# Optimization experiments

Measured on AMD Instinct MI355X. Metric: run time of the kernel, lower is better.

## Reference

```python
import jax, jax.numpy as jnp
import numpy as np
from jax import lax

STRIDES = (8, 16, 32, 64, 128)
LEVEL_HW = ((100, 128), (50, 64), (25, 32), (13, 16), (7, 8))
N, C = 16, 80
IMG_H, IMG_W = 800, 1024
THRESH = 0.05
IOU_THR = 0.6
PRE_NMS_K = 1000
POST_K = 100
CLS_OFFSET = 4096.0  # > max image coord, separates classes for batched NMS


def setup_inputs() -> dict:
    key = jax.random.key(0)
    ks = jax.random.split(key, 15)
    inp = {}
    for l, (h, w) in enumerate(LEVEL_HW):
        inp[f"cls{l}"] = jax.random.normal(ks[3 * l], (N, C, h, w), dtype=jnp.float32)
        # ltrb distances scaled to realistic pixel extents
        inp[f"reg{l}"] = jax.random.uniform(ks[3 * l + 1], (N, 4, h, w), dtype=jnp.float32) * 128.0
        inp[f"ctr{l}"] = jax.random.normal(ks[3 * l + 2], (N, 1, h, w), dtype=jnp.float32)
    return inp


def _level(cls, reg, ctr, stride):
    n, c, h, w = cls.shape
    sx = jnp.arange(w, dtype=jnp.float32) * stride + stride / 2.0
    sy = jnp.arange(h, dtype=jnp.float32) * stride + stride / 2.0
    px = jnp.broadcast_to(sx[None, :], (h, w)).reshape(-1)  # [hw]
    py = jnp.broadcast_to(sy[:, None], (h, w)).reshape(-1)  # [hw]
    # sqrt(cls_prob * centerness_prob), as in the source
    scores = jnp.sqrt(jax.nn.sigmoid(cls) * jax.nn.sigmoid(ctr))  # [n,c,h,w]
    scores = scores.transpose(0, 2, 3, 1).reshape(n, h * w, c)
    regf = reg.transpose(0, 2, 3, 1).reshape(n, h * w, 4)
    vals = scores.max(axis=-1)          # best class score per location
    labels = scores.argmax(axis=-1)
    vals = jnp.where(vals > THRESH, vals, 0.0)  # score threshold (zeroed instead of dropped)
    x1 = jnp.clip(px[None, :] - regf[..., 0], 0.0, IMG_W)
    y1 = jnp.clip(py[None, :] - regf[..., 1], 0.0, IMG_H)
    x2 = jnp.clip(px[None, :] + regf[..., 2], 0.0, IMG_W)
    y2 = jnp.clip(py[None, :] + regf[..., 3], 0.0, IMG_H)
    boxes = jnp.stack([x1, y1, x2, y2], axis=-1)  # [n,hw,4]
    return vals, labels, boxes


def _pairwise_iou(b):  # b: [K,4]
    area = (b[:, 2] - b[:, 0]) * (b[:, 3] - b[:, 1])
    lt = jnp.maximum(b[:, None, :2], b[None, :, :2])
    rb = jnp.minimum(b[:, None, 2:], b[None, :, 2:])
    wh = jnp.clip(rb - lt, 0.0)
    inter = wh[..., 0] * wh[..., 1]
    return inter / (area[:, None] + area[None, :] - inter + 1e-9)


def _nms_single(boxes, scores, labels):
    # class-aware NMS via per-class coordinate offset (torchvision batched_nms trick)
    ob = boxes + (labels.astype(boxes.dtype) * CLS_OFFSET)[:, None]
    iou = _pairwise_iou(ob)  # [K,K]
    K = boxes.shape[0]
    idxs = jnp.arange(K)

    def body(valid, i):
        keep_i = valid[i]
        valid = valid & ~(keep_i & (iou[i] > IOU_THR) & (idxs > i))
        return valid, keep_i

    _, keeps = lax.scan(body, scores > 0.0, idxs)  # greedy, scores already sorted desc
    kept_scores = jnp.where(keeps, scores, 0.0)
    top_vals, top = lax.top_k(kept_scores, POST_K)
    return boxes[top], top_vals, labels[top]


def _forward(levels):
    vals_l, labels_l, boxes_l = [], [], []
    for cls, reg, ctr, stride in levels:
        v, la, b = _level(cls, reg, ctr, stride)
        vals_l.append(v)
        labels_l.append(la)
        boxes_l.append(b)
    scores = jnp.concatenate(vals_l, axis=1)   # [N,P]
    labels = jnp.concatenate(labels_l, axis=1)  # [N,P]
    boxes = jnp.concatenate(boxes_l, axis=1)    # [N,P,4]
    tv, ti = lax.top_k(scores, PRE_NMS_K)       # pre-NMS top-k, sorted desc
    boxes_k = jnp.take_along_axis(boxes, ti[:, :, None], axis=1)
    labels_k = jnp.take_along_axis(labels, ti, axis=1)
    return jax.vmap(_nms_single)(boxes_k, tv, labels_k)


def reference(cls0, reg0, ctr0, cls1, reg1, ctr1, cls2, reg2, ctr2,
              cls3, reg3, ctr3, cls4, reg4, ctr4):
    levels = [
        (cls0, reg0, ctr0, 8), (cls1, reg1, ctr1, 16), (cls2, reg2, ctr2, 32),
        (cls3, reg3, ctr3, 64), (cls4, reg4, ctr4, 128),
    ]
    boxes, scores, labels = _forward(levels)
    return boxes, scores, labels  # [N,100,4], [N,100], [N,100]
```

## Files before the change

### kernel.cpp

```cpp
#include <hip/hip_runtime.h>
#include <stdint.h>

#pragma clang fp contract(off)

#define NB 16
#define NC 80
#define P_TOT 17064
#define P4 (P_TOT / 4)
#define PRE_K 1000
#define POST_K 100

__device__ __forceinline__ float sigmoidf_(float x) {
  return 1.0f / (1.0f + expf(-x));
}

__global__ __launch_bounds__(256, 2) void decode_kernel(
    const float* __restrict__ cls0, const float* __restrict__ reg0, const float* __restrict__ ctr0,
    const float* __restrict__ cls1, const float* __restrict__ reg1, const float* __restrict__ ctr1,
    const float* __restrict__ cls2, const float* __restrict__ reg2, const float* __restrict__ ctr2,
    const float* __restrict__ cls3, const float* __restrict__ reg3, const float* __restrict__ ctr3,
    const float* __restrict__ cls4, const float* __restrict__ reg4, const float* __restrict__ ctr4,
    int* __restrict__ labels, float* __restrict__ boxes,
    unsigned long long* __restrict__ keys)
{
  int quad = blockIdx.x * 64 + (threadIdx.x >> 2);
  int t4 = threadIdx.x & 3;
  int n = blockIdx.y;
  if (quad >= P4) return;
  int p0 = quad * 4;
  int off, wsh, hw; float stride; const float *cls, *reg, *ctr;
  if (p0 < 12800)      { off = 0;     wsh = 7; hw = 12800; stride = 8.f;   cls = cls0; reg = reg0; ctr = ctr0; }
  else if (p0 < 16000) { off = 12800; wsh = 6; hw = 3200;  stride = 16.f;  cls = cls1; reg = reg1; ctr = ctr1; }
  else if (p0 < 16800) { off = 16000; wsh = 5; hw = 800;   stride = 32.f;  cls = cls2; reg = reg2; ctr = ctr2; }
  else if (p0 < 17008) { off = 16800; wsh = 4; hw = 208;   stride = 64.f;  cls = cls3; reg = reg3; ctr = ctr3; }
  else                 { off = 17008; wsh = 3; hw = 56;    stride = 128.f; cls = cls4; reg = reg4; ctr = ctr4; }
  int loc0 = p0 - off;
  int y = loc0 >> wsh;
  int x0 = loc0 & ((1 << wsh) - 1);
  float py = (float)y * stride + 0.5f * stride;

  int c0 = t4 * 20;
  const float* cptr = cls + (size_t)n * NC * hw + (size_t)c0 * hw + loc0;
  float4 cv[20];
  #pragma unroll
  for (int k = 0; k < 20; ++k)
    cv[k] = *reinterpret_cast<const float4*>(cptr + (size_t)k * hw);

  float best[4] = { -3.4e38f, -3.4e38f, -3.4e38f, -3.4e38f };
  int bl[4] = { c0, c0, c0, c0 };
  #pragma unroll
  for (int k = 0; k < 20; ++k) {
    int c = c0 + k;
    if (cv[k].x > best[0]) { best[0] = cv[k].x; bl[0] = c; }
    if (cv[k].y > best[1]) { best[1] = cv[k].y; bl[1] = c; }
    if (cv[k].z > best[2]) { best[2] = cv[k].z; bl[2] = c; }
    if (cv[k].w > best[3]) { best[3] = cv[k].w; bl[3] = c; }
  }
  #pragma unroll
  for (int e = 0; e < 4; ++e) {
    #pragma unroll
    for (int d = 1; d <= 2; d <<= 1) {
      float ob = __shfl_xor(best[e], d);
      int ol = __shfl_xor(bl[e], d);
      if (ob > best[e] || (ob == best[e] && ol < bl[e])) { best[e] = ob; bl[e] = ol; }
    }
  }

  int e = t4;
  int loce = loc0 + e;
  float sctr_e = sigmoidf_(ctr[(size_t)n * hw + loce]);
  const float* rbase = reg + (size_t)n * 4 * hw + loce;
  float dl = rbase[0];
  float dt = rbase[(size_t)hw];
  float dr = rbase[(size_t)2 * hw];
  float db = rbase[(size_t)3 * hw];

  float s = sqrtf(sigmoidf_(best[e]) * sctr_e);
  float val = (s > 0.05f) ? s : 0.0f;
  float px = (float)(x0 + e) * stride + 0.5f * stride;
  float x1 = fminf(fmaxf(px - dl, 0.f), 1024.f);
  float y1 = fminf(fmaxf(py - dt, 0.f), 800.f);
  float x2 = fminf(fmaxf(px + dr, 0.f), 1024.f);
  float y2 = fminf(fmaxf(py + db, 0.f), 800.f);

  size_t o = (size_t)n * P_TOT + p0 + e;
  labels[o] = bl[e];
  *reinterpret_cast<float4*>(boxes + 4 * o) = make_float4(x1, y1, x2, y2);
  keys[o] = ((unsigned long long)__float_as_uint(val) << 32)
          | (unsigned long long)(0xFFFFFFFFu - (unsigned)(p0 + e));
}

__global__ __launch_bounds__(1024) void topgather_kernel(
    const unsigned long long* __restrict__ keys,
    const float* __restrict__ boxes, const int* __restrict__ labels,
    float* __restrict__ tboxes, float* __restrict__ tscores, int* __restrict__ tlabels)
{
  int n = blockIdx.x;
  int tid = threadIdx.x;
  __shared__ unsigned hist[16384];
  __shared__ unsigned A[1024];
  __shared__ unsigned s_d;
  __shared__ unsigned long long skey[2048];

  for (int i = tid; i < 16384; i += 1024) hist[i] = 0;
  skey[tid] = 0ULL;
  skey[tid + 1024] = 0ULL;
  __syncthreads();
  const unsigned long long* bk = keys + (size_t)n * P_TOT;
  for (int p = tid; p < P_TOT; p += 1024) {
    unsigned h = (unsigned)(bk[p] >> 48);
    atomicAdd(&hist[h], 1u);
  }
  __syncthreads();

  unsigned bvs[16];
  unsigned ssum = 0;
  #pragma unroll
  for (int q = 0; q < 16; ++q) { bvs[q] = hist[tid * 16 + q]; ssum += bvs[q]; }
  A[tid] = ssum;
  __syncthreads();
  for (int ofs = 1; ofs < 1024; ofs <<= 1) {
    unsigned v = A[tid];
    if (tid + ofs < 1024) v += A[tid + ofs];
    __syncthreads();
    A[tid] = v;
    __syncthreads();
  }
  unsigned An = (tid < 1023) ? A[tid + 1] : 0u;
  {
    unsigned At = A[tid];
    if (At >= PRE_K && An < PRE_K) {
      unsigned cum = An;
      int d = tid * 16;
      bool done = false;
      #pragma unroll
      for (int b = 15; b >= 0; --b) {
        if (!done) {
          cum += bvs[b];
          if (cum >= PRE_K) { d = tid * 16 + b; done = true; }
        }
      }
      s_d = (unsigned)d;
    }
  }
  __syncthreads();
  unsigned dsel = s_d;
  {
    unsigned cum = An;
    #pragma unroll
    for (int b = 15; b >= 0; --b) {
      unsigned h = (unsigned)(tid * 16 + b);
      if (h >= dsel) hist[h] = cum;
      cum += bvs[b];
    }
  }
  __syncthreads();
  for (int p = tid; p < P_TOT; p += 1024) {
    unsigned long long k = bk[p];
    unsigned h = (unsigned)(k >> 48);
    if (h >= dsel) {
      unsigned slot = atomicAdd(&hist[h], 1u);
      if (slot < 2048) skey[slot] = k;
    }
  }
  __syncthreads();
  for (int k2 = 2; k2 <= 2048; k2 <<= 1) {
    for (int j = k2 >> 1; j > 0; j >>= 1) {
      #pragma unroll
      for (int e = 0; e < 2; ++e) {
        int idx = tid + e * 1024;
        int ixj = idx ^ j;
        if (ixj > idx) {
          unsigned long long a = skey[idx], bb = skey[ixj];
          bool sw = ((idx & k2) == 0) ? (a < bb) : (a > bb);
          if (sw) { skey[idx] = bb; skey[ixj] = a; }
        }
      }
      __syncthreads();
    }
  }
  if (tid < PRE_K) {
    unsigned long long k = skey[tid];
    unsigned idx = 0xFFFFFFFFu - (unsigned)(k & 0xFFFFFFFFu);
    float sc = __uint_as_float((unsigned)(k >> 32));
    size_t src = (size_t)n * P_TOT + idx;
    size_t dst = (size_t)n * PRE_K + tid;
    tscores[dst] = sc;
    tlabels[dst] = labels[src];
    *reinterpret_cast<float4*>(tboxes + 4 * dst) =
        *reinterpret_cast<const float4*>(boxes + 4 * src);
  }
}

__global__ __launch_bounds__(128) void iou_kernel(
    const float* __restrict__ tboxes, const int* __restrict__ tlabels,
    unsigned long long* __restrict__ colsupp)
{
  int jb = blockIdx.x, w = blockIdx.y, n = blockIdx.z;
  int tid = threadIdx.x;
  int j = jb * 128 + tid;
  bool jvalid = (j < PRE_K);
  int ibase = w * 64;

  if (ibase >= jb * 128 + 128) {
    if (jvalid) colsupp[((size_t)n * PRE_K + j) * 16 + w] = 0ULL;
    return;
  }

  __shared__ float4 sb[64];
  __shared__ float sa[64];
  if (tid < 64) {
    int i = ibase + tid;
    float4 v = make_float4(0.f, 0.f, 0.f, 0.f);
    if (i < PRE_K) {
      const float* b = tboxes + ((size_t)n * PRE_K + i) * 4;
      float offv = (float)tlabels[(size_t)n * PRE_K + i] * 4096.0f;
      v = make_float4(b[0] + offv, b[1] + offv, b[2] + offv, b[3] + offv);
    }
    sb[tid] = v;
    sa[tid] = (v.z - v.x) * (v.w - v.y);
  }
  __syncthreads();

  float4 bj = make_float4(0.f, 0.f, 0.f, 0.f);
  if (jvalid) {
    const float* b = tboxes + ((size_t)n * PRE_K + j) * 4;
    float offv = (float)tlabels[(size_t)n * PRE_K + j] * 4096.0f;
    bj = make_float4(b[0] + offv, b[1] + offv, b[2] + offv, b[3] + offv);
  }
  float aj = (bj.z - bj.x) * (bj.w - bj.y);

  unsigned long long m = 0, mb = 0;
  #pragma unroll
  for (int b = 0; b < 64; ++b) {
    float4 bi = sb[b];
    float ai = sa[b];
    float lx = fmaxf(bi.x, bj.x), ly = fmaxf(bi.y, bj.y);
    float rx = fminf(bi.z, bj.z), ry = fminf(bi.w, bj.w);
    float iw = fmaxf(rx - lx, 0.f), ih = fmaxf(ry - ly, 0.f);
    float inter = iw * ih;
    float denom = ai + aj - inter + 1e-9f;
    float t = inter - 0.6f * denom;
    if (t > 0.f) m |= (1ull << b);
    if (fabsf(t) <= denom * 7.62939453125e-6f) mb |= (1ull << b);
  }
  if (mb) {
    unsigned long long r = mb;
    while (r) {
      int b = __ffsll(r) - 1; r &= r - 1;
      float4 bi = sb[b];
      float ai = sa[b];
      float lx = fmaxf(bi.x, bj.x), ly = fmaxf(bi.y, bj.y);
      float rx = fminf(bi.z, bj.z), ry = fminf(bi.w, bj.w);
      float iw = fmaxf(rx - lx, 0.f), ih = fmaxf(ry - ly, 0.f);
      float inter = iw * ih;
      float denom = ai + aj - inter + 1e-9f;
      float iou = inter / denom;
      if (iou > 0.6f) m |= (1ull << b); else m &= ~(1ull << b);
    }
  }
  unsigned long long tri;
  if (ibase >= j) tri = 0ULL;
  else if (j - ibase >= 64) tri = ~0ULL;
  else tri = (1ull << (j - ibase)) - 1ull;
  m &= tri;
  if (jvalid) colsupp[((size_t)n * PRE_K + j) * 16 + w] = m;
}

__global__ __launch_bounds__(1024) void greedyfin_kernel(
    const unsigned long long* __restrict__ colsupp, const float* __restrict__ tscores,
    const float* __restrict__ tboxes, const int* __restrict__ tlabels,
    float* __restrict__ out)
{
  int n = blockIdx.x;
  int tid = threadIdx.x;
  int wave = tid >> 6;
  int lane = tid & 63;
  __shared__ unsigned long long T[136 * 64];
  __shared__ unsigned long long keptw[16];

  {
    int wq = wave;
    int j = wq * 64 + lane;
    int base = (wq * (wq + 1)) / 2;
    if (j < PRE_K) {
      const unsigned long long* C = colsupp + ((size_t)n * PRE_K + j) * 16;
      for (int c = 0; c <= wq; ++c) T[(base + c) * 64 + lane] = C[c];
    } else {
      for (int c = 0; c <= wq; ++c) T[(base + c) * 64 + lane] = 0ULL;
    }
  }
  __syncthreads();

  if (wave == 0) {
    const float* sc = tscores + (size_t)n * PRE_K;
    float sval[16];
    #pragma unroll
    for (int k = 0; k < 16; ++k) {
      int j = k * 64 + lane;
      sval[k] = (j < PRE_K) ? sc[j] : 0.f;
    }
    unsigned removedbits = 0;
    #pragma unroll
    for (int c = 0; c < 16; ++c) {
      unsigned long long col = T[((c * (c + 1)) / 2 + c) * 64 + lane];
      unsigned long long sp = __ballot(sval[c] > 0.f);
      unsigned long long inc = __ballot(((removedbits >> c) & 1u) != 0u);
      unsigned long long K = sp & ~inc;
      unsigned long long kept = 0;
      for (int it = 0; it < 64; ++it) {
        unsigned long long Bsupp = __ballot((col & K) != 0ULL);
        unsigned long long Snew = K & ~Bsupp & ~kept;
        if (Snew == 0ULL) break;
        kept |= Snew;
        unsigned long long Bd = __ballot((col & kept) != 0ULL);
        K &= ~Bd;
      }
      if ((col & kept) != 0ULL) removedbits |= (1u << c);
      #pragma unroll
      for (int w = 0; w < 16; ++w) {
        if (w > c) {
          unsigned long long xw = T[((w * (w + 1)) / 2 + c) * 64 + lane];
          if ((xw & kept) != 0ULL) removedbits |= (1u << w);
        }
      }
      if (lane == 0) keptw[c] = kept;
    }
  }
  __syncthreads();

  __shared__ unsigned sk[1024];
  __shared__ unsigned sz[1024];
  bool inr = (tid < PRE_K);
  bool keep = inr && (((keptw[tid >> 6] >> (tid & 63)) & 1ull) != 0ull);
  sk[tid] = keep ? 1u : 0u;
  sz[tid] = (inr && !keep) ? 1u : 0u;
  __syncthreads();
  for (int ofs = 1; ofs < 1024; ofs <<= 1) {
    unsigned a = (tid >= ofs) ? sk[tid - ofs] : 0;
    unsigned b = (tid >= ofs) ? sz[tid - ofs] : 0;
    __syncthreads();
    sk[tid] += a; sz[tid] += b;
    __syncthreads();
  }
  int nk = (int)sk[1023];
  int slot = -1;
  if (inr) {
    if (keep) {
      int r = (int)sk[tid] - 1;
      if (r < POST_K) slot = r;
    } else {
      int r = nk + (int)sz[tid] - 1;
      if (r < POST_K) slot = r;
    }
  }
  if (slot >= 0) {
    size_t src = (size_t)n * PRE_K + tid;
    size_t ob = ((size_t)n * POST_K + slot) * 4;
    out[ob+0] = tboxes[4*src+0];
    out[ob+1] = tboxes[4*src+1];
    out[ob+2] = tboxes[4*src+2];
    out[ob+3] = tboxes[4*src+3];
    out[(size_t)NB*POST_K*4 + (size_t)n*POST_K + slot] = keep ? tscores[src] : 0.0f;
    out[(size_t)NB*POST_K*5 + (size_t)n*POST_K + slot] = (float)tlabels[src];
  }
}

extern "C" void kernel_launch(void* const* d_in, const int* in_sizes, int n_in,
                              void* d_out, int out_size, void* d_ws, size_t ws_size,
                              hipStream_t stream) {
  char* w = (char*)d_ws;
  auto carve = [&](size_t bytes) { char* p = w; w += (bytes + 255) & ~(size_t)255; return p; };
  int* labels   = (int*)carve((size_t)NB * P_TOT * 4);
  float* boxes  = (float*)carve((size_t)NB * P_TOT * 16);
  unsigned long long* keys = (unsigned long long*)carve((size_t)NB * P_TOT * 8);
  unsigned long long* colsupp = (unsigned long long*)carve((size_t)NB * PRE_K * 16 * 8);
  float* tboxes  = (float*)carve((size_t)NB * PRE_K * 16);
  float* tscores = (float*)carve((size_t)NB * PRE_K * 4);
  int* tlabels   = (int*)carve((size_t)NB * PRE_K * 4);

  const float* cls0 = (const float*)d_in[0];
  const float* reg0 = (const float*)d_in[1];
  const float* ctr0 = (const float*)d_in[2];
  const float* cls1 = (const float*)d_in[3];
  const float* reg1 = (const float*)d_in[4];
  const float* ctr1 = (const float*)d_in[5];
  const float* cls2 = (const float*)d_in[6];
  const float* reg2 = (const float*)d_in[7];
  const float* ctr2 = (const float*)d_in[8];
  const float* cls3 = (const float*)d_in[9];
  const float* reg3 = (const float*)d_in[10];
  const float* ctr3 = (const float*)d_in[11];
  const float* cls4 = (const float*)d_in[12];
  const float* reg4 = (const float*)d_in[13];
  const float* ctr4 = (const float*)d_in[14];

  dim3 dg((P4 + 63) / 64, NB);
  decode_kernel<<<dg, 256, 0, stream>>>(cls0, reg0, ctr0, cls1, reg1, ctr1,
                                        cls2, reg2, ctr2, cls3, reg3, ctr3,
                                        cls4, reg4, ctr4,
                                        labels, boxes, keys);
  topgather_kernel<<<NB, 1024, 0, stream>>>(keys, boxes, labels,
                                            tboxes, tscores, tlabels);
  dim3 gi(8, 16, NB);
  iou_kernel<<<gi, 128, 0, stream>>>(tboxes, tlabels, colsupp);
  greedyfin_kernel<<<NB, 1024, 0, stream>>>(colsupp, tscores, tboxes, tlabels, (float*)d_out);
}
```

Baseline: 83.05 us.

## Replace bitonic sort with bucketed rank placement and wave-shuffle scan in top-k

The top-k gather kernel now computes the histogram suffix sum with wavefront shuffles plus a tiny cross-wave step, replacing the shared-memory Hillis-Steele scan and its many barriers. The full 2048-element bitonic sort is dropped. Bucket start offsets are packed into the histogram entries, and each selected key finds its final position by counting the larger keys within its own bucket. This removes dozens of block-wide sync stages, at the risk of long serial rank loops if one bucket holds many keys, for example the zero-score bucket.

```diff
diff --git a/kernel.cpp b/kernel.cpp
--- a/kernel.cpp
+++ b/kernel.cpp
@@ -97,14 +97,14 @@
 {
   int n = blockIdx.x;
   int tid = threadIdx.x;
+  int wave = tid >> 6;
+  int lane = tid & 63;
   __shared__ unsigned hist[16384];
-  __shared__ unsigned A[1024];
-  __shared__ unsigned s_d;
+  __shared__ unsigned Wt[16], Wsuf[16];
+  __shared__ unsigned s_d, s_M;
   __shared__ unsigned long long skey[2048];
 
   for (int i = tid; i < 16384; i += 1024) hist[i] = 0;
-  skey[tid] = 0ULL;
-  skey[tid + 1024] = 0ULL;
   __syncthreads();
   const unsigned long long* bk = keys + (size_t)n * P_TOT;
   for (int p = tid; p < P_TOT; p += 1024) {
@@ -117,30 +117,42 @@
   unsigned ssum = 0;
   #pragma unroll
   for (int q = 0; q < 16; ++q) { bvs[q] = hist[tid * 16 + q]; ssum += bvs[q]; }
-  A[tid] = ssum;
-  __syncthreads();
-  for (int ofs = 1; ofs < 1024; ofs <<= 1) {
-    unsigned v = A[tid];
-    if (tid + ofs < 1024) v += A[tid + ofs];
-    __syncthreads();
-    A[tid] = v;
-    __syncthreads();
-  }
-  unsigned An = (tid < 1023) ? A[tid + 1] : 0u;
+  unsigned v = ssum;
+  #pragma unroll
+  for (int d = 1; d < 64; d <<= 1) {
+    unsigned t = __shfl_down(v, d);
+    if (lane + d < 64) v += t;
+  }
+  if (lane == 0) Wt[wave] = v;
+  __syncthreads();
+  if (wave == 0 && lane < 16) {
+    unsigned wv = Wt[lane];
+    unsigned own = wv;
+    #pragma unroll
+    for (int d = 1; d < 16; d <<= 1) {
+      unsigned t = __shfl_down(wv, d);
+      if (lane + d < 16) wv += t;
+    }
+    Wsuf[lane] = wv - own;
+  }
+  __syncthreads();
+  unsigned At = v + Wsuf[wave];
+  unsigned An = At - ssum;
   {
-    unsigned At = A[tid];
     if (At >= PRE_K && An < PRE_K) {
       unsigned cum = An;
       int d = tid * 16;
+      unsigned M = 0;
       bool done = false;
       #pragma unroll
       for (int b = 15; b >= 0; --b) {
         if (!done) {
           cum += bvs[b];
-          if (cum >= PRE_K) { d = tid * 16 + b; done = true; }
+          if (cum >= PRE_K) { d = tid * 16 + b; M = cum; done = true; }
         }
       }
       s_d = (unsigned)d;
+      s_M = M;
     }
   }
   __syncthreads();
@@ -150,7 +162,7 @@
     #pragma unroll
     for (int b = 15; b >= 0; --b) {
       unsigned h = (unsigned)(tid * 16 + b);
-      if (h >= dsel) hist[h] = cum;
+      if (h >= dsel) hist[h] = cum << 16;
       cum += bvs[b];
     }
   }
@@ -159,36 +171,38 @@
     unsigned long long k = bk[p];
     unsigned h = (unsigned)(k >> 48);
     if (h >= dsel) {
-      unsigned slot = atomicAdd(&hist[h], 1u);
+      unsigned old = atomicAdd(&hist[h], 1u);
+      unsigned slot = (old >> 16) + (old & 0xFFFFu);
       if (slot < 2048) skey[slot] = k;
     }
   }
   __syncthreads();
-  for (int k2 = 2; k2 <= 2048; k2 <<= 1) {
-    for (int j = k2 >> 1; j > 0; j >>= 1) {
-      #pragma unroll
-      for (int e = 0; e < 2; ++e) {
-        int idx = tid + e * 1024;
-        int ixj = idx ^ j;
-        if (ixj > idx) {
-          unsigned long long a = skey[idx], bb = skey[ixj];
-          bool sw = ((idx & k2) == 0) ? (a < bb) : (a > bb);
-          if (sw) { skey[idx] = bb; skey[ixj] = a; }
-        }
+  unsigned Mcap = s_M < 2048u ? s_M : 2048u;
+  #pragma unroll
+  for (int e = 0; e < 2; ++e) {
+    unsigned sidx = (unsigned)tid + e * 1024;
+    if (sidx < Mcap) {
+      unsigned long long k = skey[sidx];
+      unsigned h = (unsigned)(k >> 48);
+      unsigned info = hist[h];
+      unsigned start = info >> 16;
+      unsigned end = start + (info & 0xFFFFu);
+      if (end > 2048u) end = 2048u;
+      unsigned rank = 0;
+      for (unsigned q = start; q < end; ++q)
+        rank += (skey[q] > k) ? 1u : 0u;
+      unsigned pos = start + rank;
+      if (pos < PRE_K) {
+        unsigned idx = 0xFFFFFFFFu - (unsigned)(k & 0xFFFFFFFFu);
+        float sc = __uint_as_float((unsigned)(k >> 32));
+        size_t src = (size_t)n * P_TOT + idx;
+        size_t dst = (size_t)n * PRE_K + pos;
+        tscores[dst] = sc;
+        tlabels[dst] = labels[src];
+        *reinterpret_cast<float4*>(tboxes + 4 * dst) =
+            *reinterpret_cast<const float4*>(boxes + 4 * src);
       }
-      __syncthreads();
-    }
-  }
-  if (tid < PRE_K) {
-    unsigned long long k = skey[tid];
-    unsigned idx = 0xFFFFFFFFu - (unsigned)(k & 0xFFFFFFFFu);
-    float sc = __uint_as_float((unsigned)(k >> 32));
-    size_t src = (size_t)n * P_TOT + idx;
-    size_t dst = (size_t)n * PRE_K + tid;
-    tscores[dst] = sc;
-    tlabels[dst] = labels[src];
-    *reinterpret_cast<float4*>(tboxes + 4 * dst) =
-        *reinterpret_cast<const float4*>(boxes + 4 * src);
+    }
   }
 }
 
```

New measurement: 67.42 us. 1.23x faster.
